# Kernel tuning notes

Measured on AMD Instinct MI355X. Metric: run time of the kernel, lower is better.

Reference implementation:

```python
import jax, jax.numpy as jnp
import numpy as np

N_NODES = 50000
N_EDGES = 800000
IN_CH, HID_CH, OUT_CH = 256, 128, 64


def setup_inputs() -> dict:
    key = jax.random.key(0)
    k_x, k_e, k_w1, k_w2 = jax.random.split(key, 4)
    x = jax.random.normal(k_x, (N_NODES, IN_CH), dtype=jnp.float32)
    edge_index = jax.random.randint(k_e, (2, N_EDGES), 0, N_NODES, dtype=jnp.int32)
    # Glorot-style init like PyG GCNConv (weight [in, out], bias zeros)
    s1 = float(np.sqrt(6.0 / (IN_CH + HID_CH)))
    s2 = float(np.sqrt(6.0 / (HID_CH + OUT_CH)))
    W1 = jax.random.uniform(k_w1, (IN_CH, HID_CH), jnp.float32, -s1, s1)
    b1 = jnp.zeros((HID_CH,), jnp.float32)
    W2 = jax.random.uniform(k_w2, (HID_CH, OUT_CH), jnp.float32, -s2, s2)
    b2 = jnp.zeros((OUT_CH,), jnp.float32)
    return {"x": x, "edge_index": edge_index, "W1": W1, "b1": b1, "W2": W2, "b2": b2}


def _gcn_conv(x, src, dst, deg_inv_sqrt, W, b, n_nodes):
    """GCNConv with self-loops: D^{-1/2}(A+I)D^{-1/2} X W + b."""
    h = x @ W  # [N, out]
    norm = deg_inv_sqrt[src] * deg_inv_sqrt[dst]          # [E]
    msgs = h[src] * norm[:, None]                          # [E, out] gather
    agg = jax.ops.segment_sum(msgs, dst, num_segments=n_nodes)  # scatter-add
    self_loop = h * (deg_inv_sqrt * deg_inv_sqrt)[:, None]      # self-loop term
    return agg + self_loop + b


def reference(x, edge_index, W1, b1, W2, b2):
    n = x.shape[0]
    src, dst = edge_index[0], edge_index[1]
    # degree includes self-loop (+1), edge weight 1, counted at destination
    deg = jnp.zeros((n,), x.dtype).at[dst].add(1.0) + 1.0
    dis = jax.lax.rsqrt(deg)
    h = jax.nn.relu(_gcn_conv(x, src, dst, dis, W1, b1, n))
    out = jax.nn.relu(_gcn_conv(h, src, dst, dis, W2, b2, n))
    return out
```

## Files before the change

### kernel.cpp

```cpp
#include <hip/hip_runtime.h>

#define N_NODES 50000
#define N_EDGES 800000
#define IN_CH 256
#define HID_CH 128
#define OUT_CH 64
#define CAP 64
#define NBINS 196
#define PCHUNK 3200
#define PBLOCKS 250
#define SWZ_ELEMS (IN_CH * HID_CH + HID_CH * OUT_CH)
#define SWZ_BLOCKS (SWZ_ELEMS / 256)

typedef _Float16 f16;
typedef _Float16 f16x8 __attribute__((ext_vector_type(8)));
typedef float f32x4 __attribute__((ext_vector_type(4)));
typedef unsigned short u16;
typedef unsigned int u32;

template <int K, int N>
__device__ __forceinline__ void swz(const float* __restrict__ W, f16* __restrict__ Bsw,
                                    int idx) {
    constexpr int NTILES = N / 16;
    int j = idx & 7;
    int lane = (idx >> 3) & 63;
    int rest = idx >> 9;
    int nt = rest % NTILES;
    int ks = rest / NTILES;
    int k = ks * 32 + (lane >> 4) * 8 + j;
    int n = nt * 16 + (lane & 15);
    Bsw[idx] = (f16)W[(size_t)k * N + n];
}

__device__ __forceinline__ void scan_local(const int* __restrict__ binCnt,
                                           int* sc, int* vv) {
    const int t = threadIdx.x;
    int v = (t < NBINS) ? binCnt[t] : 0;
    sc[t] = v; vv[t] = v;
    __syncthreads();
    for (int ofs = 1; ofs < 256; ofs <<= 1) {
        int add = (t >= ofs) ? sc[t - ofs] : 0;
        __syncthreads();
        sc[t] += add;
        __syncthreads();
    }
}

__global__ __launch_bounds__(256) void k_pre(const int* __restrict__ dst,
                                             int* __restrict__ binCnt,
                                             const float* __restrict__ W1,
                                             const float* __restrict__ W2,
                                             f16* __restrict__ B1,
                                             f16* __restrict__ B2) {
    if ((int)blockIdx.x < PBLOCKS) {
        __shared__ int lcnt[NBINS];
        for (int i = threadIdx.x; i < NBINS; i += 256) lcnt[i] = 0;
        __syncthreads();
        int base = blockIdx.x * PCHUNK;
        for (int i = base + (int)threadIdx.x; i < base + PCHUNK; i += 256)
            atomicAdd(&lcnt[dst[i] >> 8], 1);
        __syncthreads();
        for (int i = threadIdx.x; i < NBINS; i += 256)
            if (lcnt[i]) atomicAdd(&binCnt[i], lcnt[i]);
        return;
    }
    int idx = ((int)blockIdx.x - PBLOCKS) * 256 + threadIdx.x;
    if (idx < IN_CH * HID_CH) {
        swz<IN_CH, HID_CH>(W1, B1, idx);
    } else {
        idx -= IN_CH * HID_CH;
        if (idx < HID_CH * OUT_CH) swz<HID_CH, OUT_CH>(W2, B2, idx);
    }
}

__global__ __launch_bounds__(256) void k_place(const int* __restrict__ src,
                                               const int* __restrict__ dst,
                                               const int* __restrict__ binCnt,
                                               int* __restrict__ binCursor,
                                               u32* __restrict__ ebuf, int E) {
    __shared__ u32 codes[PCHUNK];
    __shared__ int sc[256], vv[256];
    __shared__ int lcnt[NBINS], lbase[NBINS], lcur[NBINS];
    scan_local(binCnt, sc, vv);
    for (int i = threadIdx.x; i < NBINS; i += 256) lcnt[i] = 0;
    __syncthreads();
    int base = blockIdx.x * PCHUNK;
    int m = min(PCHUNK, E - base);
    for (int j = threadIdx.x; j < m; j += 256) {
        u32 d = (u32)dst[base + j];
        codes[j] = (d << 16) | (u32)src[base + j];
        atomicAdd(&lcnt[d >> 8], 1);
    }
    __syncthreads();
    for (int i = threadIdx.x; i < NBINS; i += 256) {
        lbase[i] = (sc[i] - vv[i]) + atomicAdd(&binCursor[i], lcnt[i]);
        lcur[i] = 0;
    }
    __syncthreads();
    for (int j = threadIdx.x; j < m; j += 256) {
        u32 c = codes[j];
        int b = c >> 24;
        int p = atomicAdd(&lcur[b], 1);
        ebuf[lbase[b] + p] = c;
    }
}

__global__ __launch_bounds__(256) void k_build(const u32* __restrict__ ebuf,
                                               const int* __restrict__ binCnt,
                                               int* __restrict__ cnt,
                                               float* __restrict__ dis,
                                               u16* __restrict__ bucket, int N) {
    __shared__ int sc[256], vv[256];
    __shared__ int lcnt[256];
    __shared__ u16 lbuck[256 * CAP];
    scan_local(binCnt, sc, vv);
    int t = threadIdx.x;
    lcnt[t] = 0;
    __syncthreads();
    int b = blockIdx.x;
    int s = sc[b] - vv[b];
    int e = sc[b];
    for (int i = s + t; i < e; i += 256) {
        u32 c = ebuf[i];
        int local = (c >> 16) & 255;
        int p = atomicAdd(&lcnt[local], 1);
        if (p < CAP) lbuck[local * CAP + p] = (u16)(c & 0xFFFFu);
    }
    __syncthreads();
    int nodeBase = b << 8;
    if (nodeBase + t < N) {
        cnt[nodeBase + t] = lcnt[t];
        dis[nodeBase + t] = rsqrtf((float)lcnt[t] + 1.0f);
    }
    const uint4* lsrc = (const uint4*)lbuck;
    uint4* gdst = (uint4*)(bucket + (size_t)nodeBase * CAP);
    for (int idx = t; idx < 256 * CAP / 8; idx += 256) {
        int row = idx >> 3;
        if (nodeBase + row < N) gdst[idx] = lsrc[idx];
    }
}

template <int K, int N, bool A_FP32, bool RELU>
__global__ __launch_bounds__(256) void k_gemm(const void* __restrict__ Av,
                                              const f16* __restrict__ Bsw,
                                              const float* __restrict__ dis,
                                              f16* __restrict__ C, int M) {
    constexpr int KSTEPS = K / 32, NTILES = N / 16;
    const int tid = threadIdx.x;
    const int wave = tid >> 6, lane = tid & 63;
    const int quad = lane >> 4, l16 = lane & 15;
    int row = blockIdx.x * 64 + wave * 16 + l16;
    const int rowc = row < M ? row : M - 1;

    f32x4 acc[NTILES];
#pragma unroll
    for (int t = 0; t < NTILES; ++t) acc[t] = (f32x4){0.f, 0.f, 0.f, 0.f};

#pragma unroll
    for (int ks = 0; ks < KSTEPS; ++ks) {
        f16x8 afrag;
        if (A_FP32) {
            const float* A = (const float*)Av;
            const float4* p = (const float4*)(A + (size_t)rowc * K + ks * 32 + quad * 8);
            float4 v0 = p[0], v1 = p[1];
            afrag[0] = (f16)v0.x; afrag[1] = (f16)v0.y;
            afrag[2] = (f16)v0.z; afrag[3] = (f16)v0.w;
            afrag[4] = (f16)v1.x; afrag[5] = (f16)v1.y;
            afrag[6] = (f16)v1.z; afrag[7] = (f16)v1.w;
        } else {
            const f16* A = (const f16*)Av;
            afrag = *(const f16x8*)(A + (size_t)rowc * K + ks * 32 + quad * 8);
            if (RELU) {
#pragma unroll
                for (int j = 0; j < 8; ++j)
                    afrag[j] = afrag[j] > (f16)0 ? afrag[j] : (f16)0;
            }
        }
#pragma unroll
        for (int t = 0; t < NTILES; ++t) {
            f16x8 bfrag = *(const f16x8*)(Bsw + (((size_t)ks * NTILES + t) * 64 + lane) * 8);
            acc[t] = __builtin_amdgcn_mfma_f32_16x16x32_f16(afrag, bfrag, acc[t], 0, 0, 0);
        }
    }

    int rbase = blockIdx.x * 64 + wave * 16 + quad * 4;
#pragma unroll
    for (int r = 0; r < 4; ++r) {
        int gr = rbase + r;
        if (gr < M) {
            float d = dis[gr];
#pragma unroll
            for (int t = 0; t < NTILES; ++t)
                C[(size_t)gr * N + t * 16 + l16] = (f16)(acc[t][r] * d);
        }
    }
}

__global__ __launch_bounds__(256) void k_pull1(const f16* __restrict__ g1,
                                               const float* __restrict__ dis,
                                               const float* __restrict__ b1,
                                               const int* __restrict__ cnt,
                                               const u16* __restrict__ bucket,
                                               f16* __restrict__ agg1) {
    int gtid = blockIdx.x * 256 + threadIdx.x;
    int u = gtid >> 4;
    int sub = gtid & 15;
    if (u >= N_NODES) return;
    const f16* gp = g1 + sub * 8;

    f16x8 sv = *(const f16x8*)(gp + (size_t)u * HID_CH);
    float a[8];
#pragma unroll
    for (int j = 0; j < 8; ++j) a[j] = (float)sv[j];

    int n = cnt[u];
    if (n > CAP) n = CAP;
    const u16* row = bucket + u * CAP;

    int k = 0;
    for (; k + 8 <= n; k += 8) {
        uint4 iv = *(const uint4*)(row + k);
        int s0 = iv.x & 0xFFFF, s1 = iv.x >> 16;
        int s2 = iv.y & 0xFFFF, s3 = iv.y >> 16;
        int s4 = iv.z & 0xFFFF, s5 = iv.z >> 16;
        int s6 = iv.w & 0xFFFF, s7 = iv.w >> 16;
        f16x8 v0 = *(const f16x8*)(gp + (size_t)s0 * HID_CH);
        f16x8 v1 = *(const f16x8*)(gp + (size_t)s1 * HID_CH);
        f16x8 v2 = *(const f16x8*)(gp + (size_t)s2 * HID_CH);
        f16x8 v3 = *(const f16x8*)(gp + (size_t)s3 * HID_CH);
        f16x8 v4 = *(const f16x8*)(gp + (size_t)s4 * HID_CH);
        f16x8 v5 = *(const f16x8*)(gp + (size_t)s5 * HID_CH);
        f16x8 v6 = *(const f16x8*)(gp + (size_t)s6 * HID_CH);
        f16x8 v7 = *(const f16x8*)(gp + (size_t)s7 * HID_CH);
#pragma unroll
        for (int j = 0; j < 8; ++j)
            a[j] += (((float)v0[j] + (float)v1[j]) + ((float)v2[j] + (float)v3[j])) +
                    (((float)v4[j] + (float)v5[j]) + ((float)v6[j] + (float)v7[j]));
    }
    if (k + 4 <= n) {
        ushort4 s4v = *(const ushort4*)(row + k);
        f16x8 v0 = *(const f16x8*)(gp + (size_t)s4v.x * HID_CH);
        f16x8 v1 = *(const f16x8*)(gp + (size_t)s4v.y * HID_CH);
        f16x8 v2 = *(const f16x8*)(gp + (size_t)s4v.z * HID_CH);
        f16x8 v3 = *(const f16x8*)(gp + (size_t)s4v.w * HID_CH);
#pragma unroll
        for (int j = 0; j < 8; ++j)
            a[j] += ((float)v0[j] + (float)v1[j]) + ((float)v2[j] + (float)v3[j]);
        k += 4;
    }
    for (; k < n; ++k) {
        f16x8 v = *(const f16x8*)(gp + (size_t)row[k] * HID_CH);
#pragma unroll
        for (int j = 0; j < 8; ++j) a[j] += (float)v[j];
    }

    float du = dis[u];
    f16x8 o;
#pragma unroll
    for (int j = 0; j < 8; ++j) o[j] = (f16)fmaf(du, a[j], b1[sub * 8 + j]);
    *(f16x8*)(agg1 + (size_t)u * HID_CH + sub * 8) = o;
}

__global__ __launch_bounds__(256) void k_pull2(const f16* __restrict__ g2,
                                               const float* __restrict__ dis,
                                               const float* __restrict__ b2,
                                               const int* __restrict__ cnt,
                                               const u16* __restrict__ bucket,
                                               float* __restrict__ out) {
    int gtid = blockIdx.x * 256 + threadIdx.x;
    int u = gtid >> 3;
    int sub = gtid & 7;
    if (u >= N_NODES) return;
    const f16* gp = g2 + sub * 8;

    f16x8 sv = *(const f16x8*)(gp + (size_t)u * OUT_CH);
    float a[8];
#pragma unroll
    for (int j = 0; j < 8; ++j) a[j] = (float)sv[j];

    int n = cnt[u];
    if (n > CAP) n = CAP;
    const u16* row = bucket + u * CAP;

    int k = 0;
    for (; k + 8 <= n; k += 8) {
        uint4 iv = *(const uint4*)(row + k);
        int s0 = iv.x & 0xFFFF, s1 = iv.x >> 16;
        int s2 = iv.y & 0xFFFF, s3 = iv.y >> 16;
        int s4 = iv.z & 0xFFFF, s5 = iv.z >> 16;
        int s6 = iv.w & 0xFFFF, s7 = iv.w >> 16;
        f16x8 v0 = *(const f16x8*)(gp + (size_t)s0 * OUT_CH);
        f16x8 v1 = *(const f16x8*)(gp + (size_t)s1 * OUT_CH);
        f16x8 v2 = *(const f16x8*)(gp + (size_t)s2 * OUT_CH);
        f16x8 v3 = *(const f16x8*)(gp + (size_t)s3 * OUT_CH);
        f16x8 v4 = *(const f16x8*)(gp + (size_t)s4 * OUT_CH);
        f16x8 v5 = *(const f16x8*)(gp + (size_t)s5 * OUT_CH);
        f16x8 v6 = *(const f16x8*)(gp + (size_t)s6 * OUT_CH);
        f16x8 v7 = *(const f16x8*)(gp + (size_t)s7 * OUT_CH);
#pragma unroll
        for (int j = 0; j < 8; ++j)
            a[j] += (((float)v0[j] + (float)v1[j]) + ((float)v2[j] + (float)v3[j])) +
                    (((float)v4[j] + (float)v5[j]) + ((float)v6[j] + (float)v7[j]));
    }
    if (k + 4 <= n) {
        ushort4 s4v = *(const ushort4*)(row + k);
        f16x8 v0 = *(const f16x8*)(gp + (size_t)s4v.x * OUT_CH);
        f16x8 v1 = *(const f16x8*)(gp + (size_t)s4v.y * OUT_CH);
        f16x8 v2 = *(const f16x8*)(gp + (size_t)s4v.z * OUT_CH);
        f16x8 v3 = *(const f16x8*)(gp + (size_t)s4v.w * OUT_CH);
#pragma unroll
        for (int j = 0; j < 8; ++j)
            a[j] += ((float)v0[j] + (float)v1[j]) + ((float)v2[j] + (float)v3[j]);
        k += 4;
    }
    for (; k < n; ++k) {
        f16x8 v = *(const f16x8*)(gp + (size_t)row[k] * OUT_CH);
#pragma unroll
        for (int j = 0; j < 8; ++j) a[j] += (float)v[j];
    }

    float du = dis[u];
    float4* op = (float4*)(out + (size_t)u * OUT_CH + sub * 8);
    float4 o0, o1;
    o0.x = fmaxf(fmaf(du, a[0], b2[sub * 8 + 0]), 0.f);
    o0.y = fmaxf(fmaf(du, a[1], b2[sub * 8 + 1]), 0.f);
    o0.z = fmaxf(fmaf(du, a[2], b2[sub * 8 + 2]), 0.f);
    o0.w = fmaxf(fmaf(du, a[3], b2[sub * 8 + 3]), 0.f);
    o1.x = fmaxf(fmaf(du, a[4], b2[sub * 8 + 4]), 0.f);
    o1.y = fmaxf(fmaf(du, a[5], b2[sub * 8 + 5]), 0.f);
    o1.z = fmaxf(fmaf(du, a[6], b2[sub * 8 + 6]), 0.f);
    o1.w = fmaxf(fmaf(du, a[7], b2[sub * 8 + 7]), 0.f);
    op[0] = o0;
    op[1] = o1;
}


extern "C" void kernel_launch(void* const* d_in, const int* in_sizes, int n_in,
                              void* d_out, int out_size, void* d_ws, size_t ws_size,
                              hipStream_t stream) {
    const float* x  = (const float*)d_in[0];
    const int* ei   = (const int*)d_in[1];
    const float* W1 = (const float*)d_in[2];
    const float* b1 = (const float*)d_in[3];
    const float* W2 = (const float*)d_in[4];
    const float* b2 = (const float*)d_in[5];
    float* out = (float*)d_out;

    const int* src = ei;
    const int* dst = ei + N_EDGES;

    char* ws = (char*)d_ws;
    size_t off = 0;
    auto alloc = [&](size_t bytes) -> void* {
        off = (off + 255) & ~(size_t)255;
        void* p = ws + off;
        off += bytes;
        return p;
    };
    int*   zbuf      = (int*)alloc((size_t)(NBINS * 2) * 4);
    int*   binCnt    = zbuf;
    int*   binCursor = zbuf + NBINS;
    u32*   ebuf      = (u32*)alloc((size_t)N_EDGES * 4);
    int*   cnt       = (int*)alloc((size_t)N_NODES * 4);
    float* dis       = (float*)alloc((size_t)N_NODES * 4);
    u16*   bucket    = (u16*)alloc((size_t)N_NODES * CAP * 2);
    f16*   W1sw      = (f16*)alloc((size_t)IN_CH * HID_CH * 2);
    f16*   W2sw      = (f16*)alloc((size_t)HID_CH * OUT_CH * 2);
    f16*   g1        = (f16*)alloc((size_t)N_NODES * HID_CH * 2);
    f16*   agg1      = (f16*)alloc((size_t)N_NODES * HID_CH * 2);
    f16*   g2        = (f16*)alloc((size_t)N_NODES * OUT_CH * 2);

    hipMemsetAsync(zbuf, 0, (size_t)(NBINS * 2) * 4, stream);

    k_pre<<<PBLOCKS + SWZ_BLOCKS, 256, 0, stream>>>(dst, binCnt, W1, W2, W1sw, W2sw);
    k_place<<<PBLOCKS, 256, 0, stream>>>(src, dst, binCnt, binCursor, ebuf, N_EDGES);
    k_build<<<NBINS, 256, 0, stream>>>(ebuf, binCnt, cnt, dis, bucket, N_NODES);

    k_gemm<IN_CH, HID_CH, true, false><<<(N_NODES + 63) / 64, 256, 0, stream>>>(
        x, W1sw, dis, g1, N_NODES);

    k_pull1<<<(N_NODES * 16 + 255) / 256, 256, 0, stream>>>(g1, dis, b1, cnt, bucket, agg1);

    k_gemm<HID_CH, OUT_CH, false, true><<<(N_NODES + 63) / 64, 256, 0, stream>>>(
        agg1, W2sw, dis, g2, N_NODES);

    k_pull2<<<(N_NODES * 8 + 255) / 256, 256, 0, stream>>>(g2, dis, b2, cnt, bucket, out);
}
```

Baseline: 198.4 us.

## Fuse bucket build with first GEMM and use per-block bin counts

The first GEMM no longer scales rows by the destination degree, so it can run in the same launch as the bucket build, with GEMM blocks and build blocks sharing one grid. The source-side normalization moves into pull1, which loads dis[src] per neighbour and applies an FMA to each message. Histogram counts are now written per block instead of accumulated with global atomics, which removes the memset and the cursor atomics. In exchange, every place and build block must sum 250 per-block counts for each bin, pull1 performs extra scattered loads of dis, and one kernel launch is saved.

```diff
diff --git a/kernel.cpp b/kernel.cpp
--- a/kernel.cpp
+++ b/kernel.cpp
@@ -11,6 +11,7 @@
 #define PBLOCKS 250
 #define SWZ_ELEMS (IN_CH * HID_CH + HID_CH * OUT_CH)
 #define SWZ_BLOCKS (SWZ_ELEMS / 256)
+#define G1B ((N_NODES + 63) / 64)
 
 typedef _Float16 f16;
 typedef _Float16 f16x8 __attribute__((ext_vector_type(8)));
@@ -32,11 +33,20 @@
     Bsw[idx] = (f16)W[(size_t)k * N + n];
 }
 
-__device__ __forceinline__ void scan_local(const int* __restrict__ binCnt,
-                                           int* sc, int* vv) {
+__device__ __forceinline__ void bin_offsets(const int* __restrict__ binCntPer,
+                                            int myBlock, int* sc, int* vv, int* lmine) {
     const int t = threadIdx.x;
-    int v = (t < NBINS) ? binCnt[t] : 0;
-    sc[t] = v; vv[t] = v;
+    int tot = 0, mine = 0;
+    if (t < NBINS) {
+        for (int b = 0; b < PBLOCKS; ++b) {
+            int v = binCntPer[b * NBINS + t];
+            tot += v;
+            if (b < myBlock) mine += v;
+        }
+    }
+    sc[t] = (t < NBINS) ? tot : 0;
+    vv[t] = sc[t];
+    if (lmine) lmine[t] = mine;
     __syncthreads();
     for (int ofs = 1; ofs < 256; ofs <<= 1) {
         int add = (t >= ofs) ? sc[t - ofs] : 0;
@@ -47,7 +57,7 @@
 }
 
 __global__ __launch_bounds__(256) void k_pre(const int* __restrict__ dst,
-                                             int* __restrict__ binCnt,
+                                             int* __restrict__ binCntPer,
                                              const float* __restrict__ W1,
                                              const float* __restrict__ W2,
                                              f16* __restrict__ B1,
@@ -61,7 +71,7 @@
             atomicAdd(&lcnt[dst[i] >> 8], 1);
         __syncthreads();
         for (int i = threadIdx.x; i < NBINS; i += 256)
-            if (lcnt[i]) atomicAdd(&binCnt[i], lcnt[i]);
+            binCntPer[blockIdx.x * NBINS + i] = lcnt[i];
         return;
     }
     int idx = ((int)blockIdx.x - PBLOCKS) * 256 + threadIdx.x;
@@ -75,29 +85,24 @@
 
 __global__ __launch_bounds__(256) void k_place(const int* __restrict__ src,
                                                const int* __restrict__ dst,
-                                               const int* __restrict__ binCnt,
-                                               int* __restrict__ binCursor,
+                                               const int* __restrict__ binCntPer,
                                                u32* __restrict__ ebuf, int E) {
     __shared__ u32 codes[PCHUNK];
-    __shared__ int sc[256], vv[256];
-    __shared__ int lcnt[NBINS], lbase[NBINS], lcur[NBINS];
-    scan_local(binCnt, sc, vv);
-    for (int i = threadIdx.x; i < NBINS; i += 256) lcnt[i] = 0;
+    __shared__ int sc[256], vv[256], lmine[256];
+    __shared__ int lbase[NBINS], lcur[NBINS];
+    bin_offsets(binCntPer, (int)blockIdx.x, sc, vv, lmine);
+    const int t = threadIdx.x;
+    if (t < NBINS) {
+        lbase[t] = (sc[t] - vv[t]) + lmine[t];
+        lcur[t] = 0;
+    }
     __syncthreads();
     int base = blockIdx.x * PCHUNK;
     int m = min(PCHUNK, E - base);
-    for (int j = threadIdx.x; j < m; j += 256) {
-        u32 d = (u32)dst[base + j];
-        codes[j] = (d << 16) | (u32)src[base + j];
-        atomicAdd(&lcnt[d >> 8], 1);
-    }
+    for (int j = t; j < m; j += 256)
+        codes[j] = ((u32)dst[base + j] << 16) | (u32)src[base + j];
     __syncthreads();
-    for (int i = threadIdx.x; i < NBINS; i += 256) {
-        lbase[i] = (sc[i] - vv[i]) + atomicAdd(&binCursor[i], lcnt[i]);
-        lcur[i] = 0;
-    }
-    __syncthreads();
-    for (int j = threadIdx.x; j < m; j += 256) {
+    for (int j = t; j < m; j += 256) {
         u32 c = codes[j];
         int b = c >> 24;
         int p = atomicAdd(&lcur[b], 1);
@@ -105,51 +110,16 @@
     }
 }
 
-__global__ __launch_bounds__(256) void k_build(const u32* __restrict__ ebuf,
-                                               const int* __restrict__ binCnt,
-                                               int* __restrict__ cnt,
-                                               float* __restrict__ dis,
-                                               u16* __restrict__ bucket, int N) {
-    __shared__ int sc[256], vv[256];
-    __shared__ int lcnt[256];
-    __shared__ u16 lbuck[256 * CAP];
-    scan_local(binCnt, sc, vv);
-    int t = threadIdx.x;
-    lcnt[t] = 0;
-    __syncthreads();
-    int b = blockIdx.x;
-    int s = sc[b] - vv[b];
-    int e = sc[b];
-    for (int i = s + t; i < e; i += 256) {
-        u32 c = ebuf[i];
-        int local = (c >> 16) & 255;
-        int p = atomicAdd(&lcnt[local], 1);
-        if (p < CAP) lbuck[local * CAP + p] = (u16)(c & 0xFFFFu);
-    }
-    __syncthreads();
-    int nodeBase = b << 8;
-    if (nodeBase + t < N) {
-        cnt[nodeBase + t] = lcnt[t];
-        dis[nodeBase + t] = rsqrtf((float)lcnt[t] + 1.0f);
-    }
-    const uint4* lsrc = (const uint4*)lbuck;
-    uint4* gdst = (uint4*)(bucket + (size_t)nodeBase * CAP);
-    for (int idx = t; idx < 256 * CAP / 8; idx += 256) {
-        int row = idx >> 3;
-        if (nodeBase + row < N) gdst[idx] = lsrc[idx];
-    }
-}
-
-template <int K, int N, bool A_FP32, bool RELU>
-__global__ __launch_bounds__(256) void k_gemm(const void* __restrict__ Av,
-                                              const f16* __restrict__ Bsw,
-                                              const float* __restrict__ dis,
-                                              f16* __restrict__ C, int M) {
+template <int K, int N, bool A_FP32, bool RELU, bool SCALE>
+__device__ __forceinline__ void gemm_body(int bid, const void* __restrict__ Av,
+                                          const f16* __restrict__ Bsw,
+                                          const float* __restrict__ dis,
+                                          f16* __restrict__ C, int M) {
     constexpr int KSTEPS = K / 32, NTILES = N / 16;
     const int tid = threadIdx.x;
     const int wave = tid >> 6, lane = tid & 63;
     const int quad = lane >> 4, l16 = lane & 15;
-    int row = blockIdx.x * 64 + wave * 16 + l16;
+    int row = bid * 64 + wave * 16 + l16;
     const int rowc = row < M ? row : M - 1;
 
     f32x4 acc[NTILES];
@@ -183,20 +153,72 @@
         }
     }
 
-    int rbase = blockIdx.x * 64 + wave * 16 + quad * 4;
+    int rbase = bid * 64 + wave * 16 + quad * 4;
 #pragma unroll
     for (int r = 0; r < 4; ++r) {
         int gr = rbase + r;
         if (gr < M) {
-            float d = dis[gr];
+            float d = SCALE ? dis[gr] : 1.0f;
 #pragma unroll
             for (int t = 0; t < NTILES; ++t)
-                C[(size_t)gr * N + t * 16 + l16] = (f16)(acc[t][r] * d);
+                C[(size_t)gr * N + t * 16 + l16] = (f16)(SCALE ? acc[t][r] * d : acc[t][r]);
         }
     }
 }
 
-__global__ __launch_bounds__(256) void k_pull1(const f16* __restrict__ g1,
+__global__ __launch_bounds__(256) void k_build_gemm1(const u32* __restrict__ ebuf,
+                                                     const int* __restrict__ binCntPer,
+                                                     int* __restrict__ cnt,
+                                                     float* __restrict__ dis,
+                                                     u16* __restrict__ bucket,
+                                                     const float* __restrict__ x,
+                                                     const f16* __restrict__ W1sw,
+                                                     f16* __restrict__ h1) {
+    __shared__ int sc[256], vv[256];
+    __shared__ int lcnt[256];
+    __shared__ u16 lbuck[256 * CAP];
+
+    if ((int)blockIdx.x < G1B) {
+        gemm_body<IN_CH, HID_CH, true, false, false>(blockIdx.x, x, W1sw, nullptr,
+                                                     h1, N_NODES);
+        return;
+    }
+    int b = (int)blockIdx.x - G1B;
+    bin_offsets(binCntPer, 0, sc, vv, nullptr);
+    int t = threadIdx.x;
+    lcnt[t] = 0;
+    __syncthreads();
+    int s = sc[b] - vv[b];
+    int e = s + vv[b];
+    for (int i = s + t; i < e; i += 256) {
+        u32 c = ebuf[i];
+        int local = (c >> 16) & 255;
+        int p = atomicAdd(&lcnt[local], 1);
+        if (p < CAP) lbuck[local * CAP + p] = (u16)(c & 0xFFFFu);
+    }
+    __syncthreads();
+    int nodeBase = b << 8;
+    if (nodeBase + t < N_NODES) {
+        cnt[nodeBase + t] = lcnt[t];
+        dis[nodeBase + t] = rsqrtf((float)lcnt[t] + 1.0f);
+    }
+    const uint4* lsrc = (const uint4*)lbuck;
+    uint4* gdst = (uint4*)(bucket + (size_t)nodeBase * CAP);
+    for (int idx = t; idx < 256 * CAP / 8; idx += 256) {
+        int row = idx >> 3;
+        if (nodeBase + row < N_NODES) gdst[idx] = lsrc[idx];
+    }
+}
+
+__global__ __launch_bounds__(256) void k_gemm2(const f16* __restrict__ agg1,
+                                               const f16* __restrict__ W2sw,
+                                               const float* __restrict__ dis,
+                                               f16* __restrict__ g2) {
+    gemm_body<HID_CH, OUT_CH, false, true, true>(blockIdx.x, agg1, W2sw, dis,
+                                                 g2, N_NODES);
+}
+
+__global__ __launch_bounds__(256) void k_pull1(const f16* __restrict__ h1,
                                                const float* __restrict__ dis,
                                                const float* __restrict__ b1,
                                                const int* __restrict__ cnt,
@@ -206,12 +228,13 @@
     int u = gtid >> 4;
     int sub = gtid & 15;
     if (u >= N_NODES) return;
-    const f16* gp = g1 + sub * 8;
-
+    const f16* gp = h1 + sub * 8;
+
+    float du = dis[u];
     f16x8 sv = *(const f16x8*)(gp + (size_t)u * HID_CH);
     float a[8];
 #pragma unroll
-    for (int j = 0; j < 8; ++j) a[j] = (float)sv[j];
+    for (int j = 0; j < 8; ++j) a[j] = du * (float)sv[j];
 
     int n = cnt[u];
     if (n > CAP) n = CAP;
@@ -224,6 +247,8 @@
         int s2 = iv.y & 0xFFFF, s3 = iv.y >> 16;
         int s4 = iv.z & 0xFFFF, s5 = iv.z >> 16;
         int s6 = iv.w & 0xFFFF, s7 = iv.w >> 16;
+        float d0 = dis[s0], d1 = dis[s1], d2 = dis[s2], d3 = dis[s3];
+        float d4 = dis[s4], d5 = dis[s5], d6 = dis[s6], d7 = dis[s7];
         f16x8 v0 = *(const f16x8*)(gp + (size_t)s0 * HID_CH);
         f16x8 v1 = *(const f16x8*)(gp + (size_t)s1 * HID_CH);
         f16x8 v2 = *(const f16x8*)(gp + (size_t)s2 * HID_CH);
@@ -233,28 +258,35 @@
         f16x8 v6 = *(const f16x8*)(gp + (size_t)s6 * HID_CH);
         f16x8 v7 = *(const f16x8*)(gp + (size_t)s7 * HID_CH);
 #pragma unroll
-        for (int j = 0; j < 8; ++j)
-            a[j] += (((float)v0[j] + (float)v1[j]) + ((float)v2[j] + (float)v3[j])) +
-                    (((float)v4[j] + (float)v5[j]) + ((float)v6[j] + (float)v7[j]));
+        for (int j = 0; j < 8; ++j) {
+            float p0 = fmaf(d0, (float)v0[j], fmaf(d1, (float)v1[j], 0.f));
+            float p1 = fmaf(d2, (float)v2[j], fmaf(d3, (float)v3[j], 0.f));
+            float p2 = fmaf(d4, (float)v4[j], fmaf(d5, (float)v5[j], 0.f));
+            float p3 = fmaf(d6, (float)v6[j], fmaf(d7, (float)v7[j], 0.f));
+            a[j] += (p0 + p1) + (p2 + p3);
+        }
     }
     if (k + 4 <= n) {
         ushort4 s4v = *(const ushort4*)(row + k);
+        float d0 = dis[s4v.x], d1 = dis[s4v.y], d2 = dis[s4v.z], d3 = dis[s4v.w];
         f16x8 v0 = *(const f16x8*)(gp + (size_t)s4v.x * HID_CH);
         f16x8 v1 = *(const f16x8*)(gp + (size_t)s4v.y * HID_CH);
         f16x8 v2 = *(const f16x8*)(gp + (size_t)s4v.z * HID_CH);
         f16x8 v3 = *(const f16x8*)(gp + (size_t)s4v.w * HID_CH);
 #pragma unroll
         for (int j = 0; j < 8; ++j)
-            a[j] += ((float)v0[j] + (float)v1[j]) + ((float)v2[j] + (float)v3[j]);
+            a[j] += fmaf(d0, (float)v0[j], fmaf(d1, (float)v1[j], 0.f)) +
+                    fmaf(d2, (float)v2[j], fmaf(d3, (float)v3[j], 0.f));
         k += 4;
     }
     for (; k < n; ++k) {
-        f16x8 v = *(const f16x8*)(gp + (size_t)row[k] * HID_CH);
-#pragma unroll
-        for (int j = 0; j < 8; ++j) a[j] += (float)v[j];
-    }
-
-    float du = dis[u];
+        int s = row[k];
+        float d = dis[s];
+        f16x8 v = *(const f16x8*)(gp + (size_t)s * HID_CH);
+#pragma unroll
+        for (int j = 0; j < 8; ++j) a[j] = fmaf(d, (float)v[j], a[j]);
+    }
+
     f16x8 o;
 #pragma unroll
     for (int j = 0; j < 8; ++j) o[j] = (f16)fmaf(du, a[j], b1[sub * 8 + j]);
@@ -357,32 +389,27 @@
         off += bytes;
         return p;
     };
-    int*   zbuf      = (int*)alloc((size_t)(NBINS * 2) * 4);
-    int*   binCnt    = zbuf;
-    int*   binCursor = zbuf + NBINS;
+    int*   binCntPer = (int*)alloc((size_t)PBLOCKS * NBINS * 4);
     u32*   ebuf      = (u32*)alloc((size_t)N_EDGES * 4);
     int*   cnt       = (int*)alloc((size_t)N_NODES * 4);
     float* dis       = (float*)alloc((size_t)N_NODES * 4);
     u16*   bucket    = (u16*)alloc((size_t)N_NODES * CAP * 2);
     f16*   W1sw      = (f16*)alloc((size_t)IN_CH * HID_CH * 2);
     f16*   W2sw      = (f16*)alloc((size_t)HID_CH * OUT_CH * 2);
-    f16*   g1        = (f16*)alloc((size_t)N_NODES * HID_CH * 2);
+    f16*   h1        = (f16*)alloc((size_t)N_NODES * HID_CH * 2);
     f16*   agg1      = (f16*)alloc((size_t)N_NODES * HID_CH * 2);
     f16*   g2        = (f16*)alloc((size_t)N_NODES * OUT_CH * 2);
 
-    hipMemsetAsync(zbuf, 0, (size_t)(NBINS * 2) * 4, stream);
-
-    k_pre<<<PBLOCKS + SWZ_BLOCKS, 256, 0, stream>>>(dst, binCnt, W1, W2, W1sw, W2sw);
-    k_place<<<PBLOCKS, 256, 0, stream>>>(src, dst, binCnt, binCursor, ebuf, N_EDGES);
-    k_build<<<NBINS, 256, 0, stream>>>(ebuf, binCnt, cnt, dis, bucket, N_NODES);
-
-    k_gemm<IN_CH, HID_CH, true, false><<<(N_NODES + 63) / 64, 256, 0, stream>>>(
-        x, W1sw, dis, g1, N_NODES);
-
-    k_pull1<<<(N_NODES * 16 + 255) / 256, 256, 0, stream>>>(g1, dis, b1, cnt, bucket, agg1);
-
-    k_gemm<HID_CH, OUT_CH, false, true><<<(N_NODES + 63) / 64, 256, 0, stream>>>(
-        agg1, W2sw, dis, g2, N_NODES);
+    k_pre<<<PBLOCKS + SWZ_BLOCKS, 256, 0, stream>>>(dst, binCntPer, W1, W2, W1sw, W2sw);
+
+    k_place<<<PBLOCKS, 256, 0, stream>>>(src, dst, binCntPer, ebuf, N_EDGES);
+
+    k_build_gemm1<<<G1B + NBINS, 256, 0, stream>>>(ebuf, binCntPer, cnt, dis, bucket,
+                                                   x, W1sw, h1);
+
+    k_pull1<<<(N_NODES * 16 + 255) / 256, 256, 0, stream>>>(h1, dis, b1, cnt, bucket, agg1);
+
+    k_gemm2<<<G1B, 256, 0, stream>>>(agg1, W2sw, dis, g2);
 
     k_pull2<<<(N_NODES * 8 + 255) / 256, 256, 0, stream>>>(g2, dis, b2, cnt, bucket, out);
 }
```

Result: slower. 202.8 us (+2.2%).

## Store hidden features in column-group-major layout for cache-local gathers

Applied to the files above, without the earlier changes.

The intermediate feature matrices g1, agg1 and g2 are stored as 16-column groups laid out group-major, so each group holds [N,16] contiguously. Pull kernels assign blocks to a single column group, so concurrent blocks gather from a smaller working set (1.6 MB per group) that fits better in L2. The GEMMs are specialised to write and read this layout, and the bucket index loads become nontemporal. The risk is that each node's bucket row and cnt are now re-read once per group, and each gather fetches only 32 bytes per row, which could hurt sector efficiency.

```diff
diff --git a/kernel.cpp b/kernel.cpp
--- a/kernel.cpp
+++ b/kernel.cpp
@@ -11,12 +11,19 @@
 #define PBLOCKS 250
 #define SWZ_ELEMS (IN_CH * HID_CH + HID_CH * OUT_CH)
 #define SWZ_BLOCKS (SWZ_ELEMS / 256)
+#define NODES_PB 128
+#define PULLB ((N_NODES + NODES_PB - 1) / NODES_PB)
 
 typedef _Float16 f16;
 typedef _Float16 f16x8 __attribute__((ext_vector_type(8)));
 typedef float f32x4 __attribute__((ext_vector_type(4)));
 typedef unsigned short u16;
 typedef unsigned int u32;
+typedef unsigned int u32x4 __attribute__((ext_vector_type(4)));
+
+static __device__ __forceinline__ u32x4 ntload4(const u16* p) {
+    return __builtin_nontemporal_load((const u32x4*)p);
+}
 
 template <int K, int N>
 __device__ __forceinline__ void swz(const float* __restrict__ W, f16* __restrict__ Bsw,
@@ -140,45 +147,32 @@
     }
 }
 
-template <int K, int N, bool A_FP32, bool RELU>
-__global__ __launch_bounds__(256) void k_gemm(const void* __restrict__ Av,
-                                              const f16* __restrict__ Bsw,
-                                              const float* __restrict__ dis,
-                                              f16* __restrict__ C, int M) {
-    constexpr int KSTEPS = K / 32, NTILES = N / 16;
+__global__ __launch_bounds__(256) void k_gemm1(const float* __restrict__ x,
+                                               const f16* __restrict__ W1sw,
+                                               const float* __restrict__ dis,
+                                               f16* __restrict__ g1T) {
     const int tid = threadIdx.x;
     const int wave = tid >> 6, lane = tid & 63;
     const int quad = lane >> 4, l16 = lane & 15;
     int row = blockIdx.x * 64 + wave * 16 + l16;
-    const int rowc = row < M ? row : M - 1;
-
-    f32x4 acc[NTILES];
-#pragma unroll
-    for (int t = 0; t < NTILES; ++t) acc[t] = (f32x4){0.f, 0.f, 0.f, 0.f};
-
-#pragma unroll
-    for (int ks = 0; ks < KSTEPS; ++ks) {
+    const int rowc = row < N_NODES ? row : N_NODES - 1;
+
+    f32x4 acc[8];
+#pragma unroll
+    for (int t = 0; t < 8; ++t) acc[t] = (f32x4){0.f, 0.f, 0.f, 0.f};
+
+#pragma unroll
+    for (int ks = 0; ks < 8; ++ks) {
+        const float4* p = (const float4*)(x + (size_t)rowc * IN_CH + ks * 32 + quad * 8);
+        float4 v0 = p[0], v1 = p[1];
         f16x8 afrag;
-        if (A_FP32) {
-            const float* A = (const float*)Av;
-            const float4* p = (const float4*)(A + (size_t)rowc * K + ks * 32 + quad * 8);
-            float4 v0 = p[0], v1 = p[1];
-            afrag[0] = (f16)v0.x; afrag[1] = (f16)v0.y;
-            afrag[2] = (f16)v0.z; afrag[3] = (f16)v0.w;
-            afrag[4] = (f16)v1.x; afrag[5] = (f16)v1.y;
-            afrag[6] = (f16)v1.z; afrag[7] = (f16)v1.w;
-        } else {
-            const f16* A = (const f16*)Av;
-            afrag = *(const f16x8*)(A + (size_t)rowc * K + ks * 32 + quad * 8);
-            if (RELU) {
-#pragma unroll
-                for (int j = 0; j < 8; ++j)
-                    afrag[j] = afrag[j] > (f16)0 ? afrag[j] : (f16)0;
-            }
-        }
-#pragma unroll
-        for (int t = 0; t < NTILES; ++t) {
-            f16x8 bfrag = *(const f16x8*)(Bsw + (((size_t)ks * NTILES + t) * 64 + lane) * 8);
+        afrag[0] = (f16)v0.x; afrag[1] = (f16)v0.y;
+        afrag[2] = (f16)v0.z; afrag[3] = (f16)v0.w;
+        afrag[4] = (f16)v1.x; afrag[5] = (f16)v1.y;
+        afrag[6] = (f16)v1.z; afrag[7] = (f16)v1.w;
+#pragma unroll
+        for (int t = 0; t < 8; ++t) {
+            f16x8 bfrag = *(const f16x8*)(W1sw + (((size_t)ks * 8 + t) * 64 + lane) * 8);
             acc[t] = __builtin_amdgcn_mfma_f32_16x16x32_f16(afrag, bfrag, acc[t], 0, 0, 0);
         }
     }
@@ -187,28 +181,28 @@
 #pragma unroll
     for (int r = 0; r < 4; ++r) {
         int gr = rbase + r;
-        if (gr < M) {
+        if (gr < N_NODES) {
             float d = dis[gr];
 #pragma unroll
-            for (int t = 0; t < NTILES; ++t)
-                C[(size_t)gr * N + t * 16 + l16] = (f16)(acc[t][r] * d);
+            for (int t = 0; t < 8; ++t)
+                g1T[((size_t)t * N_NODES + gr) * 16 + l16] = (f16)(acc[t][r] * d);
         }
     }
 }
 
-__global__ __launch_bounds__(256) void k_pull1(const f16* __restrict__ g1,
+__global__ __launch_bounds__(256) void k_pull1(const f16* __restrict__ g1T,
                                                const float* __restrict__ dis,
                                                const float* __restrict__ b1,
                                                const int* __restrict__ cnt,
                                                const u16* __restrict__ bucket,
-                                               f16* __restrict__ agg1) {
-    int gtid = blockIdx.x * 256 + threadIdx.x;
-    int u = gtid >> 4;
-    int sub = gtid & 15;
+                                               f16* __restrict__ agg1T) {
+    const int g = blockIdx.x & 7;
+    const int u = (blockIdx.x >> 3) * NODES_PB + ((int)threadIdx.x >> 1);
+    const int sub = threadIdx.x & 1;
     if (u >= N_NODES) return;
-    const f16* gp = g1 + sub * 8;
-
-    f16x8 sv = *(const f16x8*)(gp + (size_t)u * HID_CH);
+    const f16* base = g1T + (size_t)g * N_NODES * 16 + sub * 8;
+
+    f16x8 sv = *(const f16x8*)(base + (size_t)u * 16);
     float a[8];
 #pragma unroll
     for (int j = 0; j < 8; ++j) a[j] = (float)sv[j];
@@ -219,19 +213,19 @@
 
     int k = 0;
     for (; k + 8 <= n; k += 8) {
-        uint4 iv = *(const uint4*)(row + k);
+        u32x4 iv = ntload4(row + k);
         int s0 = iv.x & 0xFFFF, s1 = iv.x >> 16;
         int s2 = iv.y & 0xFFFF, s3 = iv.y >> 16;
         int s4 = iv.z & 0xFFFF, s5 = iv.z >> 16;
         int s6 = iv.w & 0xFFFF, s7 = iv.w >> 16;
-        f16x8 v0 = *(const f16x8*)(gp + (size_t)s0 * HID_CH);
-        f16x8 v1 = *(const f16x8*)(gp + (size_t)s1 * HID_CH);
-        f16x8 v2 = *(const f16x8*)(gp + (size_t)s2 * HID_CH);
-        f16x8 v3 = *(const f16x8*)(gp + (size_t)s3 * HID_CH);
-        f16x8 v4 = *(const f16x8*)(gp + (size_t)s4 * HID_CH);
-        f16x8 v5 = *(const f16x8*)(gp + (size_t)s5 * HID_CH);
-        f16x8 v6 = *(const f16x8*)(gp + (size_t)s6 * HID_CH);
-        f16x8 v7 = *(const f16x8*)(gp + (size_t)s7 * HID_CH);
+        f16x8 v0 = *(const f16x8*)(base + (size_t)s0 * 16);
+        f16x8 v1 = *(const f16x8*)(base + (size_t)s1 * 16);
+        f16x8 v2 = *(const f16x8*)(base + (size_t)s2 * 16);
+        f16x8 v3 = *(const f16x8*)(base + (size_t)s3 * 16);
+        f16x8 v4 = *(const f16x8*)(base + (size_t)s4 * 16);
+        f16x8 v5 = *(const f16x8*)(base + (size_t)s5 * 16);
+        f16x8 v6 = *(const f16x8*)(base + (size_t)s6 * 16);
+        f16x8 v7 = *(const f16x8*)(base + (size_t)s7 * 16);
 #pragma unroll
         for (int j = 0; j < 8; ++j)
             a[j] += (((float)v0[j] + (float)v1[j]) + ((float)v2[j] + (float)v3[j])) +
@@ -239,17 +233,17 @@
     }
     if (k + 4 <= n) {
         ushort4 s4v = *(const ushort4*)(row + k);
-        f16x8 v0 = *(const f16x8*)(gp + (size_t)s4v.x * HID_CH);
-        f16x8 v1 = *(const f16x8*)(gp + (size_t)s4v.y * HID_CH);
-        f16x8 v2 = *(const f16x8*)(gp + (size_t)s4v.z * HID_CH);
-        f16x8 v3 = *(const f16x8*)(gp + (size_t)s4v.w * HID_CH);
+        f16x8 v0 = *(const f16x8*)(base + (size_t)s4v.x * 16);
+        f16x8 v1 = *(const f16x8*)(base + (size_t)s4v.y * 16);
+        f16x8 v2 = *(const f16x8*)(base + (size_t)s4v.z * 16);
+        f16x8 v3 = *(const f16x8*)(base + (size_t)s4v.w * 16);
 #pragma unroll
         for (int j = 0; j < 8; ++j)
             a[j] += ((float)v0[j] + (float)v1[j]) + ((float)v2[j] + (float)v3[j]);
         k += 4;
     }
     for (; k < n; ++k) {
-        f16x8 v = *(const f16x8*)(gp + (size_t)row[k] * HID_CH);
+        f16x8 v = *(const f16x8*)(base + (size_t)row[k] * 16);
 #pragma unroll
         for (int j = 0; j < 8; ++j) a[j] += (float)v[j];
     }
@@ -257,23 +251,65 @@
     float du = dis[u];
     f16x8 o;
 #pragma unroll
-    for (int j = 0; j < 8; ++j) o[j] = (f16)fmaf(du, a[j], b1[sub * 8 + j]);
-    *(f16x8*)(agg1 + (size_t)u * HID_CH + sub * 8) = o;
-}
-
-__global__ __launch_bounds__(256) void k_pull2(const f16* __restrict__ g2,
+    for (int j = 0; j < 8; ++j) o[j] = (f16)fmaf(du, a[j], b1[g * 16 + sub * 8 + j]);
+    *(f16x8*)(agg1T + ((size_t)g * N_NODES + u) * 16 + sub * 8) = o;
+}
+
+__global__ __launch_bounds__(256) void k_gemm2(const f16* __restrict__ agg1T,
+                                               const f16* __restrict__ W2sw,
+                                               const float* __restrict__ dis,
+                                               f16* __restrict__ g2T) {
+    const int tid = threadIdx.x;
+    const int wave = tid >> 6, lane = tid & 63;
+    const int quad = lane >> 4, l16 = lane & 15;
+    int row = blockIdx.x * 64 + wave * 16 + l16;
+    const int rowc = row < N_NODES ? row : N_NODES - 1;
+
+    f32x4 acc[4];
+#pragma unroll
+    for (int t = 0; t < 4; ++t) acc[t] = (f32x4){0.f, 0.f, 0.f, 0.f};
+
+#pragma unroll
+    for (int ks = 0; ks < 4; ++ks) {
+        int gA = ks * 2 + (quad >> 1);
+        int o = (quad & 1) * 8;
+        f16x8 afrag = *(const f16x8*)(agg1T + ((size_t)gA * N_NODES + rowc) * 16 + o);
+#pragma unroll
+        for (int j = 0; j < 8; ++j)
+            afrag[j] = afrag[j] > (f16)0 ? afrag[j] : (f16)0;
+#pragma unroll
+        for (int t = 0; t < 4; ++t) {
+            f16x8 bfrag = *(const f16x8*)(W2sw + (((size_t)ks * 4 + t) * 64 + lane) * 8);
+            acc[t] = __builtin_amdgcn_mfma_f32_16x16x32_f16(afrag, bfrag, acc[t], 0, 0, 0);
+        }
+    }
+
+    int rbase = blockIdx.x * 64 + wave * 16 + quad * 4;
+#pragma unroll
+    for (int r = 0; r < 4; ++r) {
+        int gr = rbase + r;
+        if (gr < N_NODES) {
+            float d = dis[gr];
+#pragma unroll
+            for (int t = 0; t < 4; ++t)
+                g2T[((size_t)t * N_NODES + gr) * 16 + l16] = (f16)(acc[t][r] * d);
+        }
+    }
+}
+
+__global__ __launch_bounds__(256) void k_pull2(const f16* __restrict__ g2T,
                                                const float* __restrict__ dis,
                                                const float* __restrict__ b2,
                                                const int* __restrict__ cnt,
                                                const u16* __restrict__ bucket,
                                                float* __restrict__ out) {
-    int gtid = blockIdx.x * 256 + threadIdx.x;
-    int u = gtid >> 3;
-    int sub = gtid & 7;
+    const int g = blockIdx.x & 3;
+    const int u = (blockIdx.x >> 2) * NODES_PB + ((int)threadIdx.x >> 1);
+    const int sub = threadIdx.x & 1;
     if (u >= N_NODES) return;
-    const f16* gp = g2 + sub * 8;
-
-    f16x8 sv = *(const f16x8*)(gp + (size_t)u * OUT_CH);
+    const f16* base = g2T + (size_t)g * N_NODES * 16 + sub * 8;
+
+    f16x8 sv = *(const f16x8*)(base + (size_t)u * 16);
     float a[8];
 #pragma unroll
     for (int j = 0; j < 8; ++j) a[j] = (float)sv[j];
@@ -284,19 +320,19 @@
 
     int k = 0;
     for (; k + 8 <= n; k += 8) {
-        uint4 iv = *(const uint4*)(row + k);
+        u32x4 iv = ntload4(row + k);
         int s0 = iv.x & 0xFFFF, s1 = iv.x >> 16;
         int s2 = iv.y & 0xFFFF, s3 = iv.y >> 16;
         int s4 = iv.z & 0xFFFF, s5 = iv.z >> 16;
         int s6 = iv.w & 0xFFFF, s7 = iv.w >> 16;
-        f16x8 v0 = *(const f16x8*)(gp + (size_t)s0 * OUT_CH);
-        f16x8 v1 = *(const f16x8*)(gp + (size_t)s1 * OUT_CH);
-        f16x8 v2 = *(const f16x8*)(gp + (size_t)s2 * OUT_CH);
-        f16x8 v3 = *(const f16x8*)(gp + (size_t)s3 * OUT_CH);
-        f16x8 v4 = *(const f16x8*)(gp + (size_t)s4 * OUT_CH);
-        f16x8 v5 = *(const f16x8*)(gp + (size_t)s5 * OUT_CH);
-        f16x8 v6 = *(const f16x8*)(gp + (size_t)s6 * OUT_CH);
-        f16x8 v7 = *(const f16x8*)(gp + (size_t)s7 * OUT_CH);
+        f16x8 v0 = *(const f16x8*)(base + (size_t)s0 * 16);
+        f16x8 v1 = *(const f16x8*)(base + (size_t)s1 * 16);
+        f16x8 v2 = *(const f16x8*)(base + (size_t)s2 * 16);
+        f16x8 v3 = *(const f16x8*)(base + (size_t)s3 * 16);
+        f16x8 v4 = *(const f16x8*)(base + (size_t)s4 * 16);
+        f16x8 v5 = *(const f16x8*)(base + (size_t)s5 * 16);
+        f16x8 v6 = *(const f16x8*)(base + (size_t)s6 * 16);
+        f16x8 v7 = *(const f16x8*)(base + (size_t)s7 * 16);
 #pragma unroll
         for (int j = 0; j < 8; ++j)
             a[j] += (((float)v0[j] + (float)v1[j]) + ((float)v2[j] + (float)v3[j])) +
@@ -304,32 +340,33 @@
     }
     if (k + 4 <= n) {
         ushort4 s4v = *(const ushort4*)(row + k);
-        f16x8 v0 = *(const f16x8*)(gp + (size_t)s4v.x * OUT_CH);
-        f16x8 v1 = *(const f16x8*)(gp + (size_t)s4v.y * OUT_CH);
-        f16x8 v2 = *(const f16x8*)(gp + (size_t)s4v.z * OUT_CH);
-        f16x8 v3 = *(const f16x8*)(gp + (size_t)s4v.w * OUT_CH);
+        f16x8 v0 = *(const f16x8*)(base + (size_t)s4v.x * 16);
+        f16x8 v1 = *(const f16x8*)(base + (size_t)s4v.y * 16);
+        f16x8 v2 = *(const f16x8*)(base + (size_t)s4v.z * 16);
+        f16x8 v3 = *(const f16x8*)(base + (size_t)s4v.w * 16);
 #pragma unroll
         for (int j = 0; j < 8; ++j)
             a[j] += ((float)v0[j] + (float)v1[j]) + ((float)v2[j] + (float)v3[j]);
         k += 4;
     }
     for (; k < n; ++k) {
-        f16x8 v = *(const f16x8*)(gp + (size_t)row[k] * OUT_CH);
+        f16x8 v = *(const f16x8*)(base + (size_t)row[k] * 16);
 #pragma unroll
         for (int j = 0; j < 8; ++j) a[j] += (float)v[j];
     }
 
     float du = dis[u];
-    float4* op = (float4*)(out + (size_t)u * OUT_CH + sub * 8);
+    const float* bb = b2 + g * 16 + sub * 8;
+    float4* op = (float4*)(out + (size_t)u * OUT_CH + g * 16 + sub * 8);
     float4 o0, o1;
-    o0.x = fmaxf(fmaf(du, a[0], b2[sub * 8 + 0]), 0.f);
-    o0.y = fmaxf(fmaf(du, a[1], b2[sub * 8 + 1]), 0.f);
-    o0.z = fmaxf(fmaf(du, a[2], b2[sub * 8 + 2]), 0.f);
-    o0.w = fmaxf(fmaf(du, a[3], b2[sub * 8 + 3]), 0.f);
-    o1.x = fmaxf(fmaf(du, a[4], b2[sub * 8 + 4]), 0.f);
-    o1.y = fmaxf(fmaf(du, a[5], b2[sub * 8 + 5]), 0.f);
-    o1.z = fmaxf(fmaf(du, a[6], b2[sub * 8 + 6]), 0.f);
-    o1.w = fmaxf(fmaf(du, a[7], b2[sub * 8 + 7]), 0.f);
+    o0.x = fmaxf(fmaf(du, a[0], bb[0]), 0.f);
+    o0.y = fmaxf(fmaf(du, a[1], bb[1]), 0.f);
+    o0.z = fmaxf(fmaf(du, a[2], bb[2]), 0.f);
+    o0.w = fmaxf(fmaf(du, a[3], bb[3]), 0.f);
+    o1.x = fmaxf(fmaf(du, a[4], bb[4]), 0.f);
+    o1.y = fmaxf(fmaf(du, a[5], bb[5]), 0.f);
+    o1.z = fmaxf(fmaf(du, a[6], bb[6]), 0.f);
+    o1.w = fmaxf(fmaf(du, a[7], bb[7]), 0.f);
     op[0] = o0;
     op[1] = o1;
 }
@@ -366,23 +403,21 @@
     u16*   bucket    = (u16*)alloc((size_t)N_NODES * CAP * 2);
     f16*   W1sw      = (f16*)alloc((size_t)IN_CH * HID_CH * 2);
     f16*   W2sw      = (f16*)alloc((size_t)HID_CH * OUT_CH * 2);
-    f16*   g1        = (f16*)alloc((size_t)N_NODES * HID_CH * 2);
-    f16*   agg1      = (f16*)alloc((size_t)N_NODES * HID_CH * 2);
-    f16*   g2        = (f16*)alloc((size_t)N_NODES * OUT_CH * 2);
-
-    hipMemsetAsync(zbuf, 0, (size_t)(NBINS * 2) * 4, stream);
+    f16*   g1T       = (f16*)alloc((size_t)N_NODES * HID_CH * 2);
+    f16*   agg1T     = (f16*)alloc((size_t)N_NODES * HID_CH * 2);
+    f16*   g2T       = (f16*)alloc((size_t)N_NODES * OUT_CH * 2);
+
+    (void)hipMemsetAsync(zbuf, 0, (size_t)(NBINS * 2) * 4, stream);
 
     k_pre<<<PBLOCKS + SWZ_BLOCKS, 256, 0, stream>>>(dst, binCnt, W1, W2, W1sw, W2sw);
     k_place<<<PBLOCKS, 256, 0, stream>>>(src, dst, binCnt, binCursor, ebuf, N_EDGES);
     k_build<<<NBINS, 256, 0, stream>>>(ebuf, binCnt, cnt, dis, bucket, N_NODES);
 
-    k_gemm<IN_CH, HID_CH, true, false><<<(N_NODES + 63) / 64, 256, 0, stream>>>(
-        x, W1sw, dis, g1, N_NODES);
-
-    k_pull1<<<(N_NODES * 16 + 255) / 256, 256, 0, stream>>>(g1, dis, b1, cnt, bucket, agg1);
-
-    k_gemm<HID_CH, OUT_CH, false, true><<<(N_NODES + 63) / 64, 256, 0, stream>>>(
-        agg1, W2sw, dis, g2, N_NODES);
-
-    k_pull2<<<(N_NODES * 8 + 255) / 256, 256, 0, stream>>>(g2, dis, b2, cnt, bucket, out);
-}
+    k_gemm1<<<(N_NODES + 63) / 64, 256, 0, stream>>>(x, W1sw, dis, g1T);
+
+    k_pull1<<<PULLB * 8, 256, 0, stream>>>(g1T, dis, b1, cnt, bucket, agg1T);
+
+    k_gemm2<<<(N_NODES + 63) / 64, 256, 0, stream>>>(agg1T, W2sw, dis, g2T);
+
+    k_pull2<<<PULLB * 4, 256, 0, stream>>>(g2T, dis, b2, cnt, bucket, out);
+}
```

After: 241.0 us. +21.5%, slower.
